# Kernel optimization log

Hardware: AMD Instinct MI355X
Metric: run time of the kernel (lower is better)

Reference implementation:

```python
import jax, jax.numpy as jnp
import numpy as np

NR = 100000   # router nodes
NP = 200000   # packet nodes
H = 128       # h_dim
E_PASS = 600000   # router -> router
E_CONN = 600000   # packet -> router
E_TRANS = 600000  # router -> packet


def setup_inputs() -> dict:
    key = jax.random.key(0)
    ks = jax.random.split(key, 12)
    return {
        "router_feat": jax.random.normal(ks[0], (NR, H), jnp.float32),
        "packet_feat": jax.random.normal(ks[1], (NP, H), jnp.float32),
        "W_r": jax.random.normal(ks[2], (2 * H, H), jnp.float32) * 0.05,
        "b_r": jax.random.normal(ks[3], (H,), jnp.float32) * 0.05,
        "W_p": jax.random.normal(ks[4], (H, H), jnp.float32) * 0.05,
        "b_p": jax.random.normal(ks[5], (H,), jnp.float32) * 0.05,
        "pass_src": jax.random.randint(ks[6], (E_PASS,), 0, NR, jnp.int32),
        "pass_dst": jax.random.randint(ks[7], (E_PASS,), 0, NR, jnp.int32),
        "connect_src": jax.random.randint(ks[8], (E_CONN,), 0, NP, jnp.int32),
        "connect_dst": jax.random.randint(ks[9], (E_CONN,), 0, NR, jnp.int32),
        "transfer_src": jax.random.randint(ks[10], (E_TRANS,), 0, NR, jnp.int32),
        "transfer_dst": jax.random.randint(ks[11], (E_TRANS,), 0, NP, jnp.int32),
    }


def reference(router_feat, packet_feat, W_r, b_r, W_p, b_p,
              pass_src, pass_dst, connect_src, connect_dst,
              transfer_src, transfer_dst):
    # relation 'pass': router -> router, copy_u + sum -> h1 (router)
    h1_r = jax.ops.segment_sum(router_feat[pass_src], pass_dst, num_segments=NR)
    # relation 'connect': packet -> router, copy_u + sum -> h2 (router)
    h2_r = jax.ops.segment_sum(packet_feat[connect_src], connect_dst, num_segments=NR)
    # relation 'transfer': router -> packet, copy_u + mean -> h1 (packet)
    s = jax.ops.segment_sum(router_feat[transfer_src], transfer_dst, num_segments=NP)
    cnt = jax.ops.segment_sum(jnp.ones((E_TRANS,), jnp.float32), transfer_dst,
                              num_segments=NP)
    # DGL mean: zero for zero in-degree nodes
    h1_p = s / jnp.maximum(cnt, 1.0)[:, None]

    # router update: feat += ReLU(Linear(concat([h1, h2])))
    router_out = router_feat + jax.nn.relu(
        jnp.concatenate([h1_r, h2_r], axis=-1) @ W_r + b_r)
    # packet update: feat += ReLU(Linear(h1))
    packet_out = packet_feat + jax.nn.relu(h1_p @ W_p + b_p)
    return router_out, packet_out
```

## Files before the change

### kernel.cpp

```cpp
#include <hip/hip_runtime.h>

#define H_DIM 128

typedef __attribute__((ext_vector_type(8))) short short8v;
typedef __attribute__((ext_vector_type(4))) float f32x4;

__device__ __forceinline__ ushort f2bf(float f) {
  unsigned u = __builtin_bit_cast(unsigned, f);
  u += 0x7fffu + ((u >> 16) & 1u);
  return (ushort)(u >> 16);
}
__device__ __forceinline__ float bflo(unsigned u) {
  return __builtin_bit_cast(float, u << 16);
}
__device__ __forceinline__ float bfhi(unsigned u) {
  return __builtin_bit_cast(float, u & 0xffff0000u);
}

__global__ __launch_bounds__(256) void histcast_k(
    const float* __restrict__ W_r, const float* __restrict__ W_p,
    ushort* __restrict__ Wt, const int* __restrict__ d0,
    const int* __restrict__ d1, const int* __restrict__ d2,
    int* __restrict__ ro, int* __restrict__ rank, int n0, int n1, int n2,
    int NRn) {
  int bid = blockIdx.x;
  if (bid < 192) {
    int i = bid * 256 + threadIdx.x;
    int m = i >> 14;
    int j = (i >> 7) & 127;
    int k = i & 127;
    float v = (m == 0)   ? W_r[k * 128 + j]
              : (m == 1) ? W_r[(128 + k) * 128 + j]
                         : W_p[k * 128 + j];
    Wt[i] = f2bf(v);
  } else {
    int e = (bid - 192) * 256 + threadIdx.x;
    int slot;
    if (e < n0)
      slot = d0[e];
    else if (e < n0 + n1)
      slot = NRn + d1[e - n0];
    else if (e < n0 + n1 + n2)
      slot = 2 * NRn + d2[e - n0 - n1];
    else
      return;
    rank[e] = atomicAdd(&ro[slot], 1);
  }
}

__global__ __launch_bounds__(256) void scan1_k(int* __restrict__ a, int n,
                                               int* __restrict__ bsums) {
  __shared__ int ts[256];
  int t = threadIdx.x;
  int base = blockIdx.x * 2048 + t * 8;
  int v[8];
  int s = 0;
#pragma unroll
  for (int k = 0; k < 8; ++k) {
    v[k] = (base + k < n) ? a[base + k] : 0;
    s += v[k];
  }
  ts[t] = s;
  __syncthreads();
  for (int off = 1; off < 256; off <<= 1) {
    int x = (t >= off) ? ts[t - off] : 0;
    __syncthreads();
    ts[t] += x;
    __syncthreads();
  }
  if (t == 0) bsums[blockIdx.x] = ts[255];
  int run = (t == 0) ? 0 : ts[t - 1];
#pragma unroll
  for (int k = 0; k < 8; ++k) {
    int x = v[k];
    if (base + k < n) a[base + k] = run;
    run += x;
  }
}

__global__ __launch_bounds__(256) void scan23_k(int* __restrict__ a, int n,
                                                const int* __restrict__ bsums,
                                                int nb, int total) {
  __shared__ int ts[256];
  int t = threadIdx.x;
  int v = (t < nb) ? bsums[t] : 0;
  ts[t] = v;
  __syncthreads();
  for (int off = 1; off < 256; off <<= 1) {
    int x = (t >= off) ? ts[t - off] : 0;
    __syncthreads();
    ts[t] += x;
    __syncthreads();
  }
  int b = blockIdx.x;
  int excl = (b == 0) ? 0 : ts[b - 1];
  int base = b * 2048;
#pragma unroll
  for (int k = 0; k < 8; ++k) {
    int i = base + k * 256 + t;
    if (i < n) a[i] += excl;
  }
  if (b == 0 && t == 0) a[n] = total;
}

__global__ __launch_bounds__(256) void permgemm_k(
    const float* __restrict__ rf, const float* __restrict__ pf,
    const ushort* __restrict__ Wt, ushort* __restrict__ Y1,
    ushort* __restrict__ Y2, ushort* __restrict__ Yp,
    const int* __restrict__ s0a, const int* __restrict__ d0a,
    const int* __restrict__ s1a, const int* __restrict__ d1a,
    const int* __restrict__ s2a, const int* __restrict__ d2a,
    const int* __restrict__ ro, const int* __restrict__ rank,
    int* __restrict__ es, int nb1, int nb2, int M1, int M2, int n0, int n1,
    int n2, int NRn, int ng, int np) {
  __shared__ float lds_f[8192];
  long T = (long)ng + np;
  long b = blockIdx.x;
  int g_before = (int)((b * ng) / T);
  int g_incl = (int)(((b + 1) * ng) / T);
  bool do_gemm = g_incl > g_before;
  int idx = do_gemm ? g_before : (int)(b - g_before);

  if (!do_gemm) {
    long e = (long)idx * 256 + threadIdx.x;
    int src, slot;
    if (e < n0) {
      slot = d0a[e];
      src = s0a[e];
    } else if (e < n0 + n1) {
      long i = e - n0;
      slot = NRn + d1a[i];
      src = s1a[i];
    } else if (e < n0 + n1 + n2) {
      long i = e - n0 - n1;
      slot = 2 * NRn + d2a[i];
      src = s2a[i];
    } else
      return;
    es[ro[slot] + rank[e]] = src;
    return;
  }

  ushort* wl = (ushort*)lds_f;
  const float* X;
  ushort* Y;
  const ushort* Wg;
  int M, row0;
  if (idx < nb1) {
    X = rf; Y = Y1; Wg = Wt; M = M1; row0 = idx * 64;
  } else if (idx < nb1 + nb2) {
    X = pf; Y = Y2; Wg = Wt + 16384; M = M2; row0 = (idx - nb1) * 64;
  } else {
    X = rf; Y = Yp; Wg = Wt + 32768; M = M1; row0 = (idx - nb1 - nb2) * 64;
  }

  int tid = threadIdx.x;
  {
    const uint4* src = (const uint4*)Wg;
    for (int i = tid; i < 2048; i += 256) {
      int j = i >> 4;
      int k8 = (i & 15) * 8;
      int kk = k8 ^ ((j & 7) << 3);
      *(uint4*)&wl[j * 128 + kk] = src[i];
    }
  }
  __syncthreads();

  int lane = tid & 63;
  int wv = tid >> 6;
  int l15 = lane & 15;
  int kq = lane >> 4;
  int rowl = wv * 16 + l15;
  int grow = row0 + rowl;
  int growc = grow < M ? grow : M - 1;

  f32x4 acc[8];
#pragma unroll
  for (int t = 0; t < 8; ++t) {
    f32x4 z = {0.f, 0.f, 0.f, 0.f};
    acc[t] = z;
  }

#pragma unroll
  for (int ks = 0; ks < 4; ++ks) {
    int k0 = ks * 32;
    const float* ap = X + (long)growc * H_DIM + k0 + kq * 8;
    float4 a0 = *(const float4*)ap;
    float4 a1 = *(const float4*)(ap + 4);
    short8v af;
    af[0] = (short)f2bf(a0.x);
    af[1] = (short)f2bf(a0.y);
    af[2] = (short)f2bf(a0.z);
    af[3] = (short)f2bf(a0.w);
    af[4] = (short)f2bf(a1.x);
    af[5] = (short)f2bf(a1.y);
    af[6] = (short)f2bf(a1.z);
    af[7] = (short)f2bf(a1.w);
#pragma unroll
    for (int nt = 0; nt < 8; ++nt) {
      int j = nt * 16 + l15;
      int kk = (k0 + kq * 8) ^ ((j & 7) << 3);
      short8v bf = *(const short8v*)&wl[j * 128 + kk];
      acc[nt] =
          __builtin_amdgcn_mfma_f32_16x16x32_bf16(af, bf, acc[nt], 0, 0, 0);
    }
  }
  __syncthreads();
#pragma unroll
  for (int nt = 0; nt < 8; ++nt) {
#pragma unroll
    for (int r = 0; r < 4; ++r) {
      int rl = wv * 16 + kq * 4 + r;
      int col = (nt * 16 + l15) ^ (kq << 4);
      lds_f[rl * 128 + col] = acc[nt][r];
    }
  }
  __syncthreads();
  for (int i = tid; i < 2048; i += 256) {
    int flat = i * 4;
    int r = flat >> 7;
    int cc = flat & 127;
    int sw = ((r >> 2) & 3) << 4;
    float4 v = *(const float4*)&lds_f[r * 128 + (cc ^ sw)];
    int gr = row0 + r;
    if (gr < M) {
      ushort4 o;
      o.x = f2bf(v.x);
      o.y = f2bf(v.y);
      o.z = f2bf(v.z);
      o.w = f2bf(v.w);
      *(ushort4*)&Y[(long)gr * H_DIM + cc] = o;
    }
  }
}

__device__ __forceinline__ void gacc16(const ushort* __restrict__ Y,
                                       const int* __restrict__ es, int e0,
                                       int e1, int c8, float* a) {
  int e = e0;
  for (; e + 3 < e1; e += 4) {
    uint4 v0 = *(const uint4*)(Y + (long)es[e] * H_DIM + c8);
    uint4 v1 = *(const uint4*)(Y + (long)es[e + 1] * H_DIM + c8);
    uint4 v2 = *(const uint4*)(Y + (long)es[e + 2] * H_DIM + c8);
    uint4 v3 = *(const uint4*)(Y + (long)es[e + 3] * H_DIM + c8);
    a[0] += (bflo(v0.x) + bflo(v1.x)) + (bflo(v2.x) + bflo(v3.x));
    a[1] += (bfhi(v0.x) + bfhi(v1.x)) + (bfhi(v2.x) + bfhi(v3.x));
    a[2] += (bflo(v0.y) + bflo(v1.y)) + (bflo(v2.y) + bflo(v3.y));
    a[3] += (bfhi(v0.y) + bfhi(v1.y)) + (bfhi(v2.y) + bfhi(v3.y));
    a[4] += (bflo(v0.z) + bflo(v1.z)) + (bflo(v2.z) + bflo(v3.z));
    a[5] += (bfhi(v0.z) + bfhi(v1.z)) + (bfhi(v2.z) + bfhi(v3.z));
    a[6] += (bflo(v0.w) + bflo(v1.w)) + (bflo(v2.w) + bflo(v3.w));
    a[7] += (bfhi(v0.w) + bfhi(v1.w)) + (bfhi(v2.w) + bfhi(v3.w));
  }
  for (; e < e1; ++e) {
    uint4 v = *(const uint4*)(Y + (long)es[e] * H_DIM + c8);
    a[0] += bflo(v.x);
    a[1] += bfhi(v.x);
    a[2] += bflo(v.y);
    a[3] += bfhi(v.y);
    a[4] += bflo(v.z);
    a[5] += bfhi(v.z);
    a[6] += bflo(v.w);
    a[7] += bfhi(v.w);
  }
}

__global__ __launch_bounds__(256) void gather_k(
    const ushort* __restrict__ Y1, const ushort* __restrict__ Y2,
    const ushort* __restrict__ Yp, const int* __restrict__ ro,
    const int* __restrict__ es, const float* __restrict__ rf,
    const float* __restrict__ pf, const float* __restrict__ b_r,
    const float* __restrict__ b_p, float* __restrict__ out_r,
    float* __restrict__ out_p, int nrb, int NRn, int NPn) {
  int tid = threadIdx.x;
  int lane = tid & 63;
  int wv = tid >> 6;
  int sub = lane >> 4;
  int c8 = (lane & 15) * 8;
  int bid = blockIdx.x;

  float a[8] = {0.f, 0.f, 0.f, 0.f, 0.f, 0.f, 0.f, 0.f};
  if (bid < nrb) {
    int row = bid * 16 + wv * 4 + sub;
    if (row >= NRn) return;
    gacc16(Y1, es, ro[row], ro[row + 1], c8, a);
    gacc16(Y2, es, ro[NRn + row], ro[NRn + row + 1], c8, a);
    float4 bb0 = *(const float4*)&b_r[c8];
    float4 bb1 = *(const float4*)&b_r[c8 + 4];
    float bv[8] = {bb0.x, bb0.y, bb0.z, bb0.w, bb1.x, bb1.y, bb1.z, bb1.w};
    const f32x4* rp = (const f32x4*)&rf[(long)row * H_DIM + c8];
    f32x4 rv0 = __builtin_nontemporal_load(rp);
    f32x4 rv1 = __builtin_nontemporal_load(rp + 1);
    f32x4 o0, o1;
#pragma unroll
    for (int i = 0; i < 4; ++i) {
      float v = a[i] + bv[i];
      v = v > 0.f ? v : 0.f;
      o0[i] = rv0[i] + v;
      float v2 = a[i + 4] + bv[i + 4];
      v2 = v2 > 0.f ? v2 : 0.f;
      o1[i] = rv1[i] + v2;
    }
    f32x4* op = (f32x4*)&out_r[(long)row * H_DIM + c8];
    __builtin_nontemporal_store(o0, op);
    __builtin_nontemporal_store(o1, op + 1);
  } else {
    int row = (bid - nrb) * 16 + wv * 4 + sub;
    if (row >= NPn) return;
    int e0 = ro[2 * NRn + row], e1 = ro[2 * NRn + row + 1];
    gacc16(Yp, es, e0, e1, c8, a);
    int deg = e1 - e0;
    float inv = 1.0f / (float)(deg > 1 ? deg : 1);
    float4 bb0 = *(const float4*)&b_p[c8];
    float4 bb1 = *(const float4*)&b_p[c8 + 4];
    float bv[8] = {bb0.x, bb0.y, bb0.z, bb0.w, bb1.x, bb1.y, bb1.z, bb1.w};
    const f32x4* pp = (const f32x4*)&pf[(long)row * H_DIM + c8];
    f32x4 pv0 = __builtin_nontemporal_load(pp);
    f32x4 pv1 = __builtin_nontemporal_load(pp + 1);
    f32x4 o0, o1;
#pragma unroll
    for (int i = 0; i < 4; ++i) {
      float v = a[i] * inv + bv[i];
      v = v > 0.f ? v : 0.f;
      o0[i] = pv0[i] + v;
      float v2 = a[i + 4] * inv + bv[i + 4];
      v2 = v2 > 0.f ? v2 : 0.f;
      o1[i] = pv1[i] + v2;
    }
    f32x4* op = (f32x4*)&out_p[(long)row * H_DIM + c8];
    __builtin_nontemporal_store(o0, op);
    __builtin_nontemporal_store(o1, op + 1);
  }
}

extern "C" void kernel_launch(void* const* d_in, const int* in_sizes, int n_in,
                              void* d_out, int out_size, void* d_ws,
                              size_t ws_size, hipStream_t stream) {
  const float* router_feat = (const float*)d_in[0];
  const float* packet_feat = (const float*)d_in[1];
  const float* W_r = (const float*)d_in[2];
  const float* b_r = (const float*)d_in[3];
  const float* W_p = (const float*)d_in[4];
  const float* b_p = (const float*)d_in[5];
  const int* pass_src = (const int*)d_in[6];
  const int* pass_dst = (const int*)d_in[7];
  const int* connect_src = (const int*)d_in[8];
  const int* connect_dst = (const int*)d_in[9];
  const int* transfer_src = (const int*)d_in[10];
  const int* transfer_dst = (const int*)d_in[11];

  const int NRn = in_sizes[0] / H_DIM;
  const int NPn = in_sizes[1] / H_DIM;
  const int E0 = in_sizes[6], E1 = in_sizes[8], E2 = in_sizes[10];
  const long Etot = (long)E0 + E1 + E2;
  const int nseg = 2 * NRn + NPn;

  float* out_r = (float*)d_out;
  float* out_p = out_r + (size_t)NRn * H_DIM;

  int* ro = (int*)d_ws;
  int* rank = ro + (nseg + 1);
  int* es = rank + Etot;
  int* bsums = es + Etot;
  size_t int_count = (size_t)(nseg + 1) + 2 * (size_t)Etot + 256;
  size_t byte_off = ((int_count * 4) + 15) & ~(size_t)15;
  ushort* Y1 = (ushort*)((char*)d_ws + byte_off);
  ushort* Y2 = Y1 + (size_t)NRn * H_DIM;
  ushort* Yp = Y2 + (size_t)NPn * H_DIM;
  ushort* Wt = Yp + (size_t)NRn * H_DIM;

  (void)hipMemsetAsync(ro, 0, (size_t)(nseg + 1) * sizeof(int), stream);

  int egrid = (int)((Etot + 255) / 256);
  histcast_k<<<192 + egrid, 256, 0, stream>>>(W_r, W_p, Wt, pass_dst,
                                              connect_dst, transfer_dst, ro,
                                              rank, E0, E1, E2, NRn);
  int nb = (nseg + 2047) / 2048;
  scan1_k<<<nb, 256, 0, stream>>>(ro, nseg, bsums);
  scan23_k<<<nb, 256, 0, stream>>>(ro, nseg, bsums, nb, (int)Etot);

  int nb1 = (NRn + 63) / 64, nb2 = (NPn + 63) / 64, nb3 = nb1;
  int ng = nb1 + nb2 + nb3;
  int np = egrid;
  permgemm_k<<<ng + np, 256, 0, stream>>>(
      router_feat, packet_feat, Wt, Y1, Y2, Yp, pass_src, pass_dst, connect_src,
      connect_dst, transfer_src, transfer_dst, ro, rank, es, nb1, nb2, NRn, NPn,
      E0, E1, E2, NRn, ng, np);

  int nrb = (NRn + 15) / 16, npb = (NPn + 15) / 16;
  gather_k<<<nrb + npb, 256, 0, stream>>>(Y1, Y2, Yp, ro, es, router_feat,
                                          packet_feat, b_r, b_p, out_r, out_p,
                                          nrb, NRn, NPn);
}
```

Measured before the change: 321.0 us.

## Fuse both router-feature GEMMs into one block sharing the loaded A tile

The two projections of router_feat (the pass half of W_r and W_p) now run in the same block. Each router row tile is loaded and converted to bf16 once and multiplied against both weight matrices held in LDS, which removes a separate set of GEMM blocks and a second read of router_feat. The cost is double the LDS per block (64KB), which may lower occupancy, plus a second accumulator array that raises register pressure. In the gather kernel, the residual and bias loads are moved ahead of the edge gathers and the two router sums accumulate into separate arrays to increase memory-level parallelism.

```diff
diff --git a/kernel.cpp b/kernel.cpp
--- a/kernel.cpp
+++ b/kernel.cpp
@@ -111,9 +111,9 @@
     const int* __restrict__ s1a, const int* __restrict__ d1a,
     const int* __restrict__ s2a, const int* __restrict__ d2a,
     const int* __restrict__ ro, const int* __restrict__ rank,
-    int* __restrict__ es, int nb1, int nb2, int M1, int M2, int n0, int n1,
-    int n2, int NRn, int ng, int np) {
-  __shared__ float lds_f[8192];
+    int* __restrict__ es, int nbR, int M1, int M2, int n0, int n1, int n2,
+    int NRn, int ng, int np) {
+  __shared__ float lds_f[16384];
   long T = (long)ng + np;
   long b = blockIdx.x;
   int g_before = (int)((b * ng) / T);
@@ -142,26 +142,23 @@
   }
 
   ushort* wl = (ushort*)lds_f;
-  const float* X;
-  ushort* Y;
-  const ushort* Wg;
-  int M, row0;
-  if (idx < nb1) {
-    X = rf; Y = Y1; Wg = Wt; M = M1; row0 = idx * 64;
-  } else if (idx < nb1 + nb2) {
-    X = pf; Y = Y2; Wg = Wt + 16384; M = M2; row0 = (idx - nb1) * 64;
-  } else {
-    X = rf; Y = Yp; Wg = Wt + 32768; M = M1; row0 = (idx - nb1 - nb2) * 64;
-  }
-
   int tid = threadIdx.x;
+  bool is_rf = idx < nbR;
+  int row0 = (is_rf ? idx : idx - nbR) * 64;
+  int M = is_rf ? M1 : M2;
+  const float* X = is_rf ? rf : pf;
+
   {
-    const uint4* src = (const uint4*)Wg;
-    for (int i = tid; i < 2048; i += 256) {
-      int j = i >> 4;
-      int k8 = (i & 15) * 8;
+    int nmat = is_rf ? 2 : 1;
+    for (int i = tid; i < nmat * 2048; i += 256) {
+      int mat = i >> 11;
+      int w = i & 2047;
+      const uint4* src =
+          (const uint4*)(is_rf ? (mat ? Wt + 32768 : Wt) : Wt + 16384);
+      int j = w >> 4;
+      int k8 = (w & 15) * 8;
       int kk = k8 ^ ((j & 7) << 3);
-      *(uint4*)&wl[j * 128 + kk] = src[i];
+      *(uint4*)&wl[mat * 16384 + j * 128 + kk] = src[w];
     }
   }
   __syncthreads();
@@ -174,11 +171,12 @@
   int grow = row0 + rowl;
   int growc = grow < M ? grow : M - 1;
 
-  f32x4 acc[8];
+  f32x4 acc[8], acc2[8];
 #pragma unroll
   for (int t = 0; t < 8; ++t) {
     f32x4 z = {0.f, 0.f, 0.f, 0.f};
     acc[t] = z;
+    acc2[t] = z;
   }
 
 #pragma unroll
@@ -204,6 +202,16 @@
       acc[nt] =
           __builtin_amdgcn_mfma_f32_16x16x32_bf16(af, bf, acc[nt], 0, 0, 0);
     }
+    if (is_rf) {
+#pragma unroll
+      for (int nt = 0; nt < 8; ++nt) {
+        int j = nt * 16 + l15;
+        int kk = (k0 + kq * 8) ^ ((j & 7) << 3);
+        short8v bf = *(const short8v*)&wl[16384 + j * 128 + kk];
+        acc2[nt] =
+            __builtin_amdgcn_mfma_f32_16x16x32_bf16(af, bf, acc2[nt], 0, 0, 0);
+      }
+    }
   }
   __syncthreads();
 #pragma unroll
@@ -213,6 +221,7 @@
       int rl = wv * 16 + kq * 4 + r;
       int col = (nt * 16 + l15) ^ (kq << 4);
       lds_f[rl * 128 + col] = acc[nt][r];
+      if (is_rf) lds_f[8192 + rl * 128 + col] = acc2[nt][r];
     }
   }
   __syncthreads();
@@ -221,15 +230,25 @@
     int r = flat >> 7;
     int cc = flat & 127;
     int sw = ((r >> 2) & 3) << 4;
-    float4 v = *(const float4*)&lds_f[r * 128 + (cc ^ sw)];
     int gr = row0 + r;
     if (gr < M) {
+      float4 v = *(const float4*)&lds_f[r * 128 + (cc ^ sw)];
       ushort4 o;
       o.x = f2bf(v.x);
       o.y = f2bf(v.y);
       o.z = f2bf(v.z);
       o.w = f2bf(v.w);
-      *(ushort4*)&Y[(long)gr * H_DIM + cc] = o;
+      ushort* Ya = is_rf ? Y1 : Y2;
+      *(ushort4*)&Ya[(long)gr * H_DIM + cc] = o;
+      if (is_rf) {
+        float4 v2 = *(const float4*)&lds_f[8192 + r * 128 + (cc ^ sw)];
+        ushort4 o2;
+        o2.x = f2bf(v2.x);
+        o2.y = f2bf(v2.y);
+        o2.z = f2bf(v2.z);
+        o2.w = f2bf(v2.w);
+        *(ushort4*)&Yp[(long)gr * H_DIM + cc] = o2;
+      }
     }
   }
 }
@@ -279,25 +298,26 @@
   int c8 = (lane & 15) * 8;
   int bid = blockIdx.x;
 
-  float a[8] = {0.f, 0.f, 0.f, 0.f, 0.f, 0.f, 0.f, 0.f};
   if (bid < nrb) {
     int row = bid * 16 + wv * 4 + sub;
     if (row >= NRn) return;
-    gacc16(Y1, es, ro[row], ro[row + 1], c8, a);
-    gacc16(Y2, es, ro[NRn + row], ro[NRn + row + 1], c8, a);
-    float4 bb0 = *(const float4*)&b_r[c8];
-    float4 bb1 = *(const float4*)&b_r[c8 + 4];
-    float bv[8] = {bb0.x, bb0.y, bb0.z, bb0.w, bb1.x, bb1.y, bb1.z, bb1.w};
     const f32x4* rp = (const f32x4*)&rf[(long)row * H_DIM + c8];
     f32x4 rv0 = __builtin_nontemporal_load(rp);
     f32x4 rv1 = __builtin_nontemporal_load(rp + 1);
+    float4 bb0 = *(const float4*)&b_r[c8];
+    float4 bb1 = *(const float4*)&b_r[c8 + 4];
+    float a[8] = {0.f, 0.f, 0.f, 0.f, 0.f, 0.f, 0.f, 0.f};
+    float c[8] = {0.f, 0.f, 0.f, 0.f, 0.f, 0.f, 0.f, 0.f};
+    gacc16(Y1, es, ro[row], ro[row + 1], c8, a);
+    gacc16(Y2, es, ro[NRn + row], ro[NRn + row + 1], c8, c);
+    float bv[8] = {bb0.x, bb0.y, bb0.z, bb0.w, bb1.x, bb1.y, bb1.z, bb1.w};
     f32x4 o0, o1;
 #pragma unroll
     for (int i = 0; i < 4; ++i) {
-      float v = a[i] + bv[i];
+      float v = (a[i] + c[i]) + bv[i];
       v = v > 0.f ? v : 0.f;
       o0[i] = rv0[i] + v;
-      float v2 = a[i + 4] + bv[i + 4];
+      float v2 = (a[i + 4] + c[i + 4]) + bv[i + 4];
       v2 = v2 > 0.f ? v2 : 0.f;
       o1[i] = rv1[i] + v2;
     }
@@ -307,16 +327,17 @@
   } else {
     int row = (bid - nrb) * 16 + wv * 4 + sub;
     if (row >= NPn) return;
+    const f32x4* pp = (const f32x4*)&pf[(long)row * H_DIM + c8];
+    f32x4 pv0 = __builtin_nontemporal_load(pp);
+    f32x4 pv1 = __builtin_nontemporal_load(pp + 1);
+    float4 bb0 = *(const float4*)&b_p[c8];
+    float4 bb1 = *(const float4*)&b_p[c8 + 4];
     int e0 = ro[2 * NRn + row], e1 = ro[2 * NRn + row + 1];
+    float a[8] = {0.f, 0.f, 0.f, 0.f, 0.f, 0.f, 0.f, 0.f};
     gacc16(Yp, es, e0, e1, c8, a);
     int deg = e1 - e0;
     float inv = 1.0f / (float)(deg > 1 ? deg : 1);
-    float4 bb0 = *(const float4*)&b_p[c8];
-    float4 bb1 = *(const float4*)&b_p[c8 + 4];
     float bv[8] = {bb0.x, bb0.y, bb0.z, bb0.w, bb1.x, bb1.y, bb1.z, bb1.w};
-    const f32x4* pp = (const f32x4*)&pf[(long)row * H_DIM + c8];
-    f32x4 pv0 = __builtin_nontemporal_load(pp);
-    f32x4 pv1 = __builtin_nontemporal_load(pp + 1);
     f32x4 o0, o1;
 #pragma unroll
     for (int i = 0; i < 4; ++i) {
@@ -379,13 +400,13 @@
   scan1_k<<<nb, 256, 0, stream>>>(ro, nseg, bsums);
   scan23_k<<<nb, 256, 0, stream>>>(ro, nseg, bsums, nb, (int)Etot);
 
-  int nb1 = (NRn + 63) / 64, nb2 = (NPn + 63) / 64, nb3 = nb1;
-  int ng = nb1 + nb2 + nb3;
+  int nbR = (NRn + 63) / 64, nbP = (NPn + 63) / 64;
+  int ng = nbR + nbP;
   int np = egrid;
   permgemm_k<<<ng + np, 256, 0, stream>>>(
       router_feat, packet_feat, Wt, Y1, Y2, Yp, pass_src, pass_dst, connect_src,
-      connect_dst, transfer_src, transfer_dst, ro, rank, es, nb1, nb2, NRn, NPn,
-      E0, E1, E2, NRn, ng, np);
+      connect_dst, transfer_src, transfer_dst, ro, rank, es, nbR, NRn, NPn, E0,
+      E1, E2, NRn, ng, np);
 
   int nrb = (NRn + 15) / 16, npb = (NPn + 15) / 16;
   gather_k<<<nrb + npb, 256, 0, stream>>>(Y1, Y2, Yp, ro, es, router_feat,
```

New measurement: 357.9 us. +11.5%, slower.

## Process 128 rows per GEMM block and hoist residual loads in gather

Applied to the files above, without the earlier changes.

The projection GEMM blocks now compute two 64-row tiles each, reusing the LDS-staged bf16 weight slice across both and halving the number of blocks that reload weights. Each wave keeps two accumulator sets, which raises register pressure and may lower occupancy. The gather kernel issues the residual and bias loads before the neighbour accumulation so they overlap with it, and accumulates the two router relations into separate arrays for more independent adds.

```diff
diff --git a/kernel.cpp b/kernel.cpp
--- a/kernel.cpp
+++ b/kernel.cpp
@@ -15,6 +15,18 @@
 }
 __device__ __forceinline__ float bfhi(unsigned u) {
   return __builtin_bit_cast(float, u & 0xffff0000u);
+}
+__device__ __forceinline__ short8v pack_bf8(float4 a0, float4 a1) {
+  short8v af;
+  af[0] = (short)f2bf(a0.x);
+  af[1] = (short)f2bf(a0.y);
+  af[2] = (short)f2bf(a0.z);
+  af[3] = (short)f2bf(a0.w);
+  af[4] = (short)f2bf(a1.x);
+  af[5] = (short)f2bf(a1.y);
+  af[6] = (short)f2bf(a1.z);
+  af[7] = (short)f2bf(a1.w);
+  return af;
 }
 
 __global__ __launch_bounds__(256) void histcast_k(
@@ -147,11 +159,11 @@
   const ushort* Wg;
   int M, row0;
   if (idx < nb1) {
-    X = rf; Y = Y1; Wg = Wt; M = M1; row0 = idx * 64;
+    X = rf; Y = Y1; Wg = Wt; M = M1; row0 = idx * 128;
   } else if (idx < nb1 + nb2) {
-    X = pf; Y = Y2; Wg = Wt + 16384; M = M2; row0 = (idx - nb1) * 64;
+    X = pf; Y = Y2; Wg = Wt + 16384; M = M2; row0 = (idx - nb1) * 128;
   } else {
-    X = rf; Y = Yp; Wg = Wt + 32768; M = M1; row0 = (idx - nb1 - nb2) * 64;
+    X = rf; Y = Yp; Wg = Wt + 32768; M = M1; row0 = (idx - nb1 - nb2) * 128;
   }
 
   int tid = threadIdx.x;
@@ -171,40 +183,42 @@
   int l15 = lane & 15;
   int kq = lane >> 4;
   int rowl = wv * 16 + l15;
-  int grow = row0 + rowl;
-  int growc = grow < M ? grow : M - 1;
-
-  f32x4 acc[8];
+  int g0 = row0 + rowl;
+  int g1 = row0 + 64 + rowl;
+  int gc0 = g0 < M ? g0 : M - 1;
+  int gc1 = g1 < M ? g1 : M - 1;
+
+  f32x4 acc0[8], acc1[8];
 #pragma unroll
   for (int t = 0; t < 8; ++t) {
     f32x4 z = {0.f, 0.f, 0.f, 0.f};
-    acc[t] = z;
+    acc0[t] = z;
+    acc1[t] = z;
   }
 
 #pragma unroll
   for (int ks = 0; ks < 4; ++ks) {
     int k0 = ks * 32;
-    const float* ap = X + (long)growc * H_DIM + k0 + kq * 8;
-    float4 a0 = *(const float4*)ap;
-    float4 a1 = *(const float4*)(ap + 4);
-    short8v af;
-    af[0] = (short)f2bf(a0.x);
-    af[1] = (short)f2bf(a0.y);
-    af[2] = (short)f2bf(a0.z);
-    af[3] = (short)f2bf(a0.w);
-    af[4] = (short)f2bf(a1.x);
-    af[5] = (short)f2bf(a1.y);
-    af[6] = (short)f2bf(a1.z);
-    af[7] = (short)f2bf(a1.w);
+    const float* ap0 = X + (long)gc0 * H_DIM + k0 + kq * 8;
+    const float* ap1 = X + (long)gc1 * H_DIM + k0 + kq * 8;
+    float4 a00 = *(const float4*)ap0;
+    float4 a01 = *(const float4*)(ap0 + 4);
+    float4 a10 = *(const float4*)ap1;
+    float4 a11 = *(const float4*)(ap1 + 4);
+    short8v af0 = pack_bf8(a00, a01);
+    short8v af1 = pack_bf8(a10, a11);
 #pragma unroll
     for (int nt = 0; nt < 8; ++nt) {
       int j = nt * 16 + l15;
       int kk = (k0 + kq * 8) ^ ((j & 7) << 3);
       short8v bf = *(const short8v*)&wl[j * 128 + kk];
-      acc[nt] =
-          __builtin_amdgcn_mfma_f32_16x16x32_bf16(af, bf, acc[nt], 0, 0, 0);
-    }
-  }
+      acc0[nt] =
+          __builtin_amdgcn_mfma_f32_16x16x32_bf16(af0, bf, acc0[nt], 0, 0, 0);
+      acc1[nt] =
+          __builtin_amdgcn_mfma_f32_16x16x32_bf16(af1, bf, acc1[nt], 0, 0, 0);
+    }
+  }
+
   __syncthreads();
 #pragma unroll
   for (int nt = 0; nt < 8; ++nt) {
@@ -212,7 +226,7 @@
     for (int r = 0; r < 4; ++r) {
       int rl = wv * 16 + kq * 4 + r;
       int col = (nt * 16 + l15) ^ (kq << 4);
-      lds_f[rl * 128 + col] = acc[nt][r];
+      lds_f[rl * 128 + col] = acc0[nt][r];
     }
   }
   __syncthreads();
@@ -221,9 +235,36 @@
     int r = flat >> 7;
     int cc = flat & 127;
     int sw = ((r >> 2) & 3) << 4;
-    float4 v = *(const float4*)&lds_f[r * 128 + (cc ^ sw)];
     int gr = row0 + r;
     if (gr < M) {
+      float4 v = *(const float4*)&lds_f[r * 128 + (cc ^ sw)];
+      ushort4 o;
+      o.x = f2bf(v.x);
+      o.y = f2bf(v.y);
+      o.z = f2bf(v.z);
+      o.w = f2bf(v.w);
+      *(ushort4*)&Y[(long)gr * H_DIM + cc] = o;
+    }
+  }
+  __syncthreads();
+#pragma unroll
+  for (int nt = 0; nt < 8; ++nt) {
+#pragma unroll
+    for (int r = 0; r < 4; ++r) {
+      int rl = wv * 16 + kq * 4 + r;
+      int col = (nt * 16 + l15) ^ (kq << 4);
+      lds_f[rl * 128 + col] = acc1[nt][r];
+    }
+  }
+  __syncthreads();
+  for (int i = tid; i < 2048; i += 256) {
+    int flat = i * 4;
+    int r = flat >> 7;
+    int cc = flat & 127;
+    int sw = ((r >> 2) & 3) << 4;
+    int gr = row0 + 64 + r;
+    if (gr < M) {
+      float4 v = *(const float4*)&lds_f[r * 128 + (cc ^ sw)];
       ushort4 o;
       o.x = f2bf(v.x);
       o.y = f2bf(v.y);
@@ -279,25 +320,26 @@
   int c8 = (lane & 15) * 8;
   int bid = blockIdx.x;
 
-  float a[8] = {0.f, 0.f, 0.f, 0.f, 0.f, 0.f, 0.f, 0.f};
   if (bid < nrb) {
     int row = bid * 16 + wv * 4 + sub;
     if (row >= NRn) return;
-    gacc16(Y1, es, ro[row], ro[row + 1], c8, a);
-    gacc16(Y2, es, ro[NRn + row], ro[NRn + row + 1], c8, a);
-    float4 bb0 = *(const float4*)&b_r[c8];
-    float4 bb1 = *(const float4*)&b_r[c8 + 4];
-    float bv[8] = {bb0.x, bb0.y, bb0.z, bb0.w, bb1.x, bb1.y, bb1.z, bb1.w};
     const f32x4* rp = (const f32x4*)&rf[(long)row * H_DIM + c8];
     f32x4 rv0 = __builtin_nontemporal_load(rp);
     f32x4 rv1 = __builtin_nontemporal_load(rp + 1);
+    float4 bb0 = *(const float4*)&b_r[c8];
+    float4 bb1 = *(const float4*)&b_r[c8 + 4];
+    float a[8] = {0.f, 0.f, 0.f, 0.f, 0.f, 0.f, 0.f, 0.f};
+    float c[8] = {0.f, 0.f, 0.f, 0.f, 0.f, 0.f, 0.f, 0.f};
+    gacc16(Y1, es, ro[row], ro[row + 1], c8, a);
+    gacc16(Y2, es, ro[NRn + row], ro[NRn + row + 1], c8, c);
+    float bv[8] = {bb0.x, bb0.y, bb0.z, bb0.w, bb1.x, bb1.y, bb1.z, bb1.w};
     f32x4 o0, o1;
 #pragma unroll
     for (int i = 0; i < 4; ++i) {
-      float v = a[i] + bv[i];
+      float v = (a[i] + c[i]) + bv[i];
       v = v > 0.f ? v : 0.f;
       o0[i] = rv0[i] + v;
-      float v2 = a[i + 4] + bv[i + 4];
+      float v2 = (a[i + 4] + c[i + 4]) + bv[i + 4];
       v2 = v2 > 0.f ? v2 : 0.f;
       o1[i] = rv1[i] + v2;
     }
@@ -307,16 +349,17 @@
   } else {
     int row = (bid - nrb) * 16 + wv * 4 + sub;
     if (row >= NPn) return;
+    const f32x4* pp = (const f32x4*)&pf[(long)row * H_DIM + c8];
+    f32x4 pv0 = __builtin_nontemporal_load(pp);
+    f32x4 pv1 = __builtin_nontemporal_load(pp + 1);
+    float4 bb0 = *(const float4*)&b_p[c8];
+    float4 bb1 = *(const float4*)&b_p[c8 + 4];
     int e0 = ro[2 * NRn + row], e1 = ro[2 * NRn + row + 1];
+    float a[8] = {0.f, 0.f, 0.f, 0.f, 0.f, 0.f, 0.f, 0.f};
     gacc16(Yp, es, e0, e1, c8, a);
     int deg = e1 - e0;
     float inv = 1.0f / (float)(deg > 1 ? deg : 1);
-    float4 bb0 = *(const float4*)&b_p[c8];
-    float4 bb1 = *(const float4*)&b_p[c8 + 4];
     float bv[8] = {bb0.x, bb0.y, bb0.z, bb0.w, bb1.x, bb1.y, bb1.z, bb1.w};
-    const f32x4* pp = (const f32x4*)&pf[(long)row * H_DIM + c8];
-    f32x4 pv0 = __builtin_nontemporal_load(pp);
-    f32x4 pv1 = __builtin_nontemporal_load(pp + 1);
     f32x4 o0, o1;
 #pragma unroll
     for (int i = 0; i < 4; ++i) {
@@ -379,7 +422,7 @@
   scan1_k<<<nb, 256, 0, stream>>>(ro, nseg, bsums);
   scan23_k<<<nb, 256, 0, stream>>>(ro, nseg, bsums, nb, (int)Etot);
 
-  int nb1 = (NRn + 63) / 64, nb2 = (NPn + 63) / 64, nb3 = nb1;
+  int nb1 = (NRn + 127) / 128, nb2 = (NPn + 127) / 128, nb3 = nb1;
   int ng = nb1 + nb2 + nb3;
   int np = egrid;
   permgemm_k<<<ng + np, 256, 0, stream>>>(
```

Measured after the change: 319.9 us. Within noise of the previous version (-0.3%).
